# Kernel optimization log

Hardware: AMD Instinct MI355X
Metric: run time of the kernel (lower is better)

Reference implementation:

```python
import jax, jax.numpy as jnp
import numpy as np

B, T, N_MODEL, HEAD_SIZE = 8, 4096, 1024, 128


def setup_inputs() -> dict:
    key = jax.random.key(0)
    k1, k2 = jax.random.split(key)
    x = jax.random.normal(k1, (B, T, N_MODEL), dtype=jnp.float32)
    W_K = jax.random.normal(k2, (HEAD_SIZE, N_MODEL), dtype=jnp.float32) * 0.02
    return {"x": x, "W_K": W_K}


def _rope_inplace_semantics(t, cos, sin):
    """Replicates the source's in-place slice writes:
    even' = t1*cos + t2*sin  (written first)
    odd'  = -even'*sin + t2*cos  (t1 view already holds even' when read)
    """
    t1 = t[..., ::2]
    t2 = t[..., 1::2]
    even = t1 * cos + t2 * sin
    odd = -even * sin + t2 * cos
    # re-interleave: [..., half, 2] -> [..., head_size]
    return jnp.stack([even, odd], axis=-1).reshape(t.shape)


def reference(x, W_K):
    head_size = W_K.shape[0]
    T_len = x.shape[-2]
    half = head_size // 2
    # frequency-only thetas (no position index, as in source)
    thetas = jnp.power(10000.0, -(jnp.arange(half, dtype=jnp.float32) / half))
    cos = jnp.cos(thetas)
    sin = jnp.sin(thetas)

    # NOTE: source uses self.K for k, q AND v (faithful to the bug)
    k = x @ W_K.T  # [B, T, head_size]
    v = k
    k_rot = _rope_inplace_semantics(k, cos, sin)
    q_rot = k_rot  # q computed identically from K(x)

    # w[i,j] = k_i . q_j (k first, as in source einsum)
    w = jnp.einsum('bik,bjk->bij', k_rot, q_rot) * (head_size ** -0.5)
    mask = jnp.triu(jnp.full((T_len, T_len), -jnp.inf, dtype=w.dtype), k=1)
    w = jax.nn.softmax(w + mask, axis=-1)
    out = jnp.einsum('bij,bjk->bik', w, v)  # [B, T, head_size]
    return out
```

## Files before the change

### kernel.cpp

```cpp
#include <hip/hip_runtime.h>
#include <hip/hip_bf16.h>
#include <cstdint>

typedef __attribute__((ext_vector_type(8))) __bf16 bf16x8;
typedef __attribute__((ext_vector_type(4))) float f32x4;
typedef __attribute__((ext_vector_type(16))) float f32x16;

typedef const __attribute__((address_space(1))) void* as1cvp;
typedef __attribute__((address_space(3))) void* as3vp;

__device__ __forceinline__ void gload_lds16(const void* g, void* l) {
  __builtin_amdgcn_global_load_lds((as1cvp)g, (as3vp)l, 16, 0, 0);
}
__device__ __forceinline__ float readlane_f(float v, int l) {
  return __uint_as_float((uint32_t)__builtin_amdgcn_readlane((int)__float_as_uint(v), l));
}

#define KSCALE 0.3570962f
#define SMBIAS 24.0f

__device__ __forceinline__ int vperm(int p) {
  return 16 * (p >> 4) + 4 * ((p >> 3) & 1) + 8 * ((p >> 2) & 1) + (p & 3);
}

__global__ __launch_bounds__(256) void wk_convert_kernel(
    const float* __restrict__ wk, __bf16* __restrict__ wkbf) {
  int i = (blockIdx.x * 256 + threadIdx.x) * 4;
  f32x4 v = *(const f32x4*)(wk + i);
  union { __bf16 e[4]; uint64_t u; } p;
#pragma unroll
  for (int j = 0; j < 4; j++) p.e[j] = (__bf16)v[j];
  *(uint64_t*)(wkbf + i) = p.u;
}

__global__ __launch_bounds__(256, 4) void proj_rope_kernel(
    const float* __restrict__ x, const __bf16* __restrict__ wkbf,
    __bf16* __restrict__ k2, __bf16* __restrict__ vt3)
{
  __shared__ __align__(16) char psmem[40960];
  const int tid = threadIdx.x;
  const int wid = tid >> 6;
  const int lane = tid & 63;
  const int m0 = blockIdx.x * 32;
  const int wn = wid * 32;

  f32x4 acc[2][2];
#pragma unroll
  for (int i = 0; i < 2; i++)
#pragma unroll
    for (int j = 0; j < 2; j++) acc[i][j] = (f32x4)0.f;

  const int ar = tid >> 3, ac = (tid & 7) * 8;
  const float* gx0 = x + (size_t)(m0 + ar) * 1024 + ac;

  f32x4 pa0, pa1;
#define LOADA(K0) do { const float* gp = gx0 + (K0); pa0 = *(const f32x4*)gp; pa1 = *(const f32x4*)(gp + 4); } while (0)
#define WRITEA(BUF) do { \
    bf16x8 av; \
    _Pragma("unroll") for (int jj = 0; jj < 4; jj++) { av[jj] = (__bf16)pa0[jj]; av[4 + jj] = (__bf16)pa1[jj]; } \
    *(bf16x8*)((__bf16*)psmem + (BUF) * 2048 + ar * 64 + (ac ^ ((ar & 7) << 3))) = av; \
  } while (0)
#define STAGEB(BUF, K0) do { \
    _Pragma("unroll") for (int h = 0; h < 4; h++) { \
      int Lc = tid + h * 256; int row = Lc >> 3, sp = Lc & 7; \
      gload_lds16((const char*)wkbf + row * 2048 + (K0) * 2 + ((sp ^ (row & 7)) << 4), \
                  psmem + 8192 + (BUF) * 16384 + Lc * 16); \
    } } while (0)

  LOADA(0);
  STAGEB(0, 0);
  WRITEA(0);
  __syncthreads();

  for (int t = 0; t < 16; t++) {
    const int buf = t & 1;
    const bool more = (t + 1 < 16);
    if (more) { LOADA((t + 1) * 64); STAGEB(buf ^ 1, (t + 1) * 64); }
    const __bf16* As = (const __bf16*)psmem + buf * 2048;
    const __bf16* Bs = (const __bf16*)(psmem + 8192 + buf * 16384);
#pragma unroll
    for (int kk = 0; kk < 2; kk++) {
      bf16x8 afr[2], bfr[2];
#pragma unroll
      for (int mi = 0; mi < 2; mi++) {
        int row = mi * 16 + (lane & 15);
        int col = (kk * 32 + (lane >> 4) * 8) ^ ((row & 7) << 3);
        afr[mi] = *(const bf16x8*)&As[row * 64 + col];
      }
#pragma unroll
      for (int ni = 0; ni < 2; ni++) {
        int row = wn + ni * 16 + (lane & 15);
        int col = (kk * 32 + (lane >> 4) * 8) ^ ((row & 7) << 3);
        bfr[ni] = *(const bf16x8*)&Bs[row * 64 + col];
      }
#pragma unroll
      for (int mi = 0; mi < 2; mi++)
#pragma unroll
        for (int ni = 0; ni < 2; ni++)
          acc[mi][ni] = __builtin_amdgcn_mfma_f32_16x16x32_bf16(afr[mi], bfr[ni], acc[mi][ni], 0, 0, 0);
    }
    if (more) WRITEA(buf ^ 1);
    __syncthreads();
  }

  float cosv[2], sinv[2];
#pragma unroll
  for (int ni = 0; ni < 2; ni++) {
    int d = wn + ni * 16 + (lane & 15);
    float theta = exp2f((float)(d >> 1) * -0.20762050593046014f);
    cosv[ni] = cosf(theta);
    sinv[ni] = sinf(theta);
  }
  __bf16* vl = (__bf16*)psmem;
  __bf16* kl_e = (__bf16*)(psmem + 8192);
  const bool evenlane = ((lane & 1) == 0);
#pragma unroll
  for (int mi = 0; mi < 2; mi++) {
#pragma unroll
    for (int r = 0; r < 4; r++) {
      int ml = mi * 16 + (lane >> 4) * 4 + r;
#pragma unroll
      for (int ni = 0; ni < 2; ni++) {
        float val = acc[mi][ni][r];
        int d = wn + ni * 16 + (lane & 15);
        vl[ml * 128 + d] = (__bf16)val;
        float partner = __shfl_xor(val, 1);
        float e = evenlane ? val : partner;
        float o = evenlane ? partner : val;
        float ev = e * cosv[ni] + o * sinv[ni];
        float od = -ev * sinv[ni] + o * cosv[ni];
        float kr = evenlane ? ev : od;
        kl_e[ml * 128 + (d ^ ((ml & 15) << 3))] = (__bf16)(kr * KSCALE);
      }
    }
  }
  __syncthreads();
  const size_t T = blockIdx.x;
  {
    int s = tid >> 4, kvb = tid & 15;
    __bf16* kg = k2 + T * 4096 + s * 256;
#pragma unroll
    for (int h = 0; h < 2; h++) {
      int kv = kvb + h * 16;
      bf16x8 w = *(const bf16x8*)&kl_e[kv * 128 + ((s * 8) ^ ((kv & 15) << 3))];
      *(bf16x8*)(kg + kv * 8) = w;
    }
  }
  {
    int d = tid >> 1, th = tid & 1;
    __bf16* vg = vt3 + T * 4096 + d * 8;
#pragma unroll
    for (int cc = 0; cc < 2; cc++) {
      int c = 2 * th + cc;
      bf16x8 w;
#pragma unroll
      for (int jj = 0; jj < 8; jj++)
        w[jj] = vl[vperm(c * 8 + jj) * 128 + d];
      *(bf16x8*)(vg + c * 1024) = w;
    }
  }
}

__global__ __launch_bounds__(128) void attn_kernel(
    const __bf16* __restrict__ k2, const __bf16* __restrict__ vt3,
    float* __restrict__ out)
{
  __shared__ __align__(16) char smem[16512];
  const int tid = threadIdx.x;
  const int split = tid >> 6;
  const int lane = tid & 63;
  const int lo5 = lane & 31;
  const int hi = lane >> 5;
  const int b = blockIdx.x & 7;
  const int i = (int)(blockIdx.x >> 3);
  const int qb = (i < 64) ? (127 - i) : (i - 64);
  const int q0 = qb * 32;
  const int jd = qb;
  const __bf16* kt = k2 + (size_t)b * 524288;
  const __bf16* vb = vt3 + (size_t)b * 524288;

  bf16x8 qf[8];
  {
    const __bf16* qp = kt + (size_t)qb * 4096 + lo5 * 8;
#pragma unroll
    for (int ks = 0; ks < 8; ks++) qf[ks] = *(const bf16x8*)(qp + (2 * ks + hi) * 256);
  }

  f32x16 acc[4];
#pragma unroll
  for (int dt = 0; dt < 4; dt++) acc[dt] = (f32x16)0.f;
  float l_r = 0.f;

  for (int j = split; j <= jd; j += 2) {
    const __bf16* kp = kt + (size_t)j * 4096 + lo5 * 8;
    const __bf16* vp = vb + (size_t)j * 4096 + lo5 * 8;
    bf16x8 kf[8];
#pragma unroll
    for (int ks = 0; ks < 8; ks++) kf[ks] = *(const bf16x8*)(kp + (2 * ks + hi) * 256);
    bf16x8 vf0[4], vf1[4];
#pragma unroll
    for (int dt = 0; dt < 4; dt++) {
      vf0[dt] = *(const bf16x8*)(vp + hi * 1024 + dt * 256);
      vf1[dt] = *(const bf16x8*)(vp + (2 + hi) * 1024 + dt * 256);
    }
    f32x16 S = (f32x16)(-SMBIAS);
    __builtin_amdgcn_s_setprio(1);
#pragma unroll
    for (int ks = 0; ks < 8; ks++)
      S = __builtin_amdgcn_mfma_f32_32x32x16_bf16(kf[ks], qf[ks], S, 0, 0, 0);
    __builtin_amdgcn_s_setprio(0);
    if (j == jd) {
      const int kv0 = j * 32;
#pragma unroll
      for (int r = 0; r < 16; r++) {
        int kvg = kv0 + (r & 3) + 8 * (r >> 2) + 4 * hi;
        if (kvg > q0 + lo5) S[r] = -1e30f;
      }
    }
    union U { __bf16 e[8]; bf16x8 v; };
    U pk0, pk1;
    float rs = 0.f;
#pragma unroll
    for (int jj = 0; jj < 8; jj++) { float p = exp2f(S[jj]); rs += p; pk0.e[jj] = (__bf16)p; }
#pragma unroll
    for (int jj = 0; jj < 8; jj++) { float p = exp2f(S[8 + jj]); rs += p; pk1.e[jj] = (__bf16)p; }
    l_r += rs;
    __builtin_amdgcn_s_setprio(1);
#pragma unroll
    for (int dt = 0; dt < 4; dt++)
      acc[dt] = __builtin_amdgcn_mfma_f32_32x32x16_bf16(pk0.v, vf0[dt], acc[dt], 0, 0, 0);
#pragma unroll
    for (int dt = 0; dt < 4; dt++)
      acc[dt] = __builtin_amdgcn_mfma_f32_32x32x16_bf16(pk1.v, vf1[dt], acc[dt], 0, 0, 0);
    __builtin_amdgcn_s_setprio(0);
  }
  l_r += __shfl_xor(l_r, 32);

  float* mreg = (float*)smem;
  float* lbuf = (float*)(smem + 16384);
  if (split == 1) {
#pragma unroll
    for (int r = 0; r < 16; r++) {
      int ql = (r & 3) + 8 * (r >> 2) + 4 * hi;
#pragma unroll
      for (int dt = 0; dt < 4; dt++) mreg[ql * 128 + dt * 32 + lo5] = acc[dt][r];
    }
    if (lane < 32) lbuf[lane] = l_r;
  }
  __syncthreads();
  if (split == 0) {
    float invl = 1.0f / (l_r + lbuf[lo5]);
    float* ob = out + (size_t)b * 4096 * 128;
#pragma unroll
    for (int r = 0; r < 16; r++) {
      const int rb = (r & 3) + 8 * (r >> 2);
      float ivr = hi ? readlane_f(invl, rb + 4) : readlane_f(invl, rb);
      const int ql = rb + 4 * hi;
      const size_t qg = (size_t)(q0 + ql);
#pragma unroll
      for (int dt = 0; dt < 4; dt++) {
        float ov = (acc[dt][r] + mreg[ql * 128 + dt * 32 + lo5]) * ivr;
        ob[qg * 128 + dt * 32 + lo5] = ov;
      }
    }
  }
}

extern "C" void kernel_launch(void* const* d_in, const int* in_sizes, int n_in,
                              void* d_out, int out_size, void* d_ws, size_t ws_size,
                              hipStream_t stream) {
  const float* x  = (const float*)d_in[0];
  const float* wk = (const float*)d_in[1];
  __bf16* k2  = (__bf16*)d_ws;
  __bf16* vt3 = k2 + (size_t)8 * 4096 * 128;
  float* out  = (float*)d_out;
  __bf16* wkbf = (__bf16*)d_out;
  wk_convert_kernel<<<128, 256, 0, stream>>>(wk, wkbf);
  proj_rope_kernel<<<1024, 256, 0, stream>>>(x, wkbf, k2, vt3);
  attn_kernel<<<1024, 128, 0, stream>>>(k2, vt3, out);
}
```

Measured before the change: 98.15 us.

## Share K/V tiles across two query blocks via double-buffered LDS staging

The attention kernel now processes 64 query rows per workgroup (four waves: two query sub-blocks times two KV splits) and stages K and V tiles into LDS with async global-to-LDS loads, double-buffered across iterations. Each staged K/V tile is reused by both query sub-blocks, halving global K/V traffic, and the next tile is prefetched while the current one is consumed. The QK^T MFMA chain is split into two independent accumulators to shorten dependency latency. It adds a workgroup barrier per iteration and 64KB of LDS, which lowers occupancy and makes waves wait on each other.

```diff
diff --git a/kernel.cpp b/kernel.cpp
--- a/kernel.cpp
+++ b/kernel.cpp
@@ -161,29 +161,30 @@
   }
 }
 
-__global__ __launch_bounds__(128) void attn_kernel(
+__global__ __launch_bounds__(256) void attn_kernel(
     const __bf16* __restrict__ k2, const __bf16* __restrict__ vt3,
     float* __restrict__ out)
 {
-  __shared__ __align__(16) char smem[16512];
+  __shared__ __align__(16) char smem[65536];
   const int tid = threadIdx.x;
-  const int split = tid >> 6;
+  const int wid = tid >> 6;
   const int lane = tid & 63;
   const int lo5 = lane & 31;
   const int hi = lane >> 5;
   const int b = blockIdx.x & 7;
   const int i = (int)(blockIdx.x >> 3);
-  const int qb = (i < 64) ? (127 - i) : (i - 64);
-  const int q0 = qb * 32;
-  const int jd = qb;
-  const __bf16* kt = k2 + (size_t)b * 524288;
-  const __bf16* vb = vt3 + (size_t)b * 524288;
+  const int qb = (i < 32) ? (63 - i) : (i - 32);
+  const int sub = wid >> 1, split = wid & 1;
+  const int q0 = qb * 64 + sub * 32;
+  const int jd = 2 * qb + sub;
+  const char* kbc = (const char*)(k2 + (size_t)b * 524288);
+  const char* vbc = (const char*)(vt3 + (size_t)b * 524288);
 
   bf16x8 qf[8];
   {
-    const __bf16* qp = kt + (size_t)qb * 4096 + lo5 * 8;
-#pragma unroll
-    for (int ks = 0; ks < 8; ks++) qf[ks] = *(const bf16x8*)(qp + (2 * ks + hi) * 256);
+    const char* qp = kbc + (size_t)(2 * qb + sub) * 8192 + lo5 * 16;
+#pragma unroll
+    for (int ks = 0; ks < 8; ks++) qf[ks] = *(const bf16x8*)(qp + (2 * ks + hi) * 512);
   }
 
   f32x16 acc[4];
@@ -191,53 +192,78 @@
   for (int dt = 0; dt < 4; dt++) acc[dt] = (f32x16)0.f;
   float l_r = 0.f;
 
-  for (int j = split; j <= jd; j += 2) {
-    const __bf16* kp = kt + (size_t)j * 4096 + lo5 * 8;
-    const __bf16* vp = vb + (size_t)j * 4096 + lo5 * 8;
-    bf16x8 kf[8];
-#pragma unroll
-    for (int ks = 0; ks < 8; ks++) kf[ks] = *(const bf16x8*)(kp + (2 * ks + hi) * 256);
-    bf16x8 vf0[4], vf1[4];
-#pragma unroll
-    for (int dt = 0; dt < 4; dt++) {
-      vf0[dt] = *(const bf16x8*)(vp + hi * 1024 + dt * 256);
-      vf1[dt] = *(const bf16x8*)(vp + (2 + hi) * 1024 + dt * 256);
-    }
-    f32x16 S = (f32x16)(-SMBIAS);
-    __builtin_amdgcn_s_setprio(1);
-#pragma unroll
-    for (int ks = 0; ks < 8; ks++)
-      S = __builtin_amdgcn_mfma_f32_32x32x16_bf16(kf[ks], qf[ks], S, 0, 0, 0);
-    __builtin_amdgcn_s_setprio(0);
-    if (j == jd) {
-      const int kv0 = j * 32;
-#pragma unroll
-      for (int r = 0; r < 16; r++) {
-        int kvg = kv0 + (r & 3) + 8 * (r >> 2) + 4 * hi;
-        if (kvg > q0 + lo5) S[r] = -1e30f;
-      }
-    }
-    union U { __bf16 e[8]; bf16x8 v; };
-    U pk0, pk1;
-    float rs = 0.f;
-#pragma unroll
-    for (int jj = 0; jj < 8; jj++) { float p = exp2f(S[jj]); rs += p; pk0.e[jj] = (__bf16)p; }
-#pragma unroll
-    for (int jj = 0; jj < 8; jj++) { float p = exp2f(S[8 + jj]); rs += p; pk1.e[jj] = (__bf16)p; }
-    l_r += rs;
-    __builtin_amdgcn_s_setprio(1);
-#pragma unroll
-    for (int dt = 0; dt < 4; dt++)
-      acc[dt] = __builtin_amdgcn_mfma_f32_32x32x16_bf16(pk0.v, vf0[dt], acc[dt], 0, 0, 0);
-#pragma unroll
-    for (int dt = 0; dt < 4; dt++)
-      acc[dt] = __builtin_amdgcn_mfma_f32_32x32x16_bf16(pk1.v, vf1[dt], acc[dt], 0, 0, 0);
-    __builtin_amdgcn_s_setprio(0);
+#define STAGE(BSEL, JP) do { \
+    _Pragma("unroll") \
+    for (int t = 0; t < 2; t++) { \
+      const char* ks_ = kbc + (size_t)((JP) * 2 + t) * 8192; \
+      const char* vs_ = vbc + (size_t)((JP) * 2 + t) * 8192; \
+      char* dst_ = smem + (BSEL) * 32768 + t * 16384; \
+      _Pragma("unroll") \
+      for (int h = 0; h < 2; h++) { \
+        gload_lds16(ks_ + (tid + h * 256) * 16, dst_ + (tid + h * 256) * 16); \
+        gload_lds16(vs_ + (tid + h * 256) * 16, dst_ + 8192 + (tid + h * 256) * 16); \
+      } \
+    } \
+  } while (0)
+
+  const int nj = qb + 1;
+  STAGE(0, 0);
+  __syncthreads();
+
+  for (int jp = 0; jp < nj; jp++) {
+    if (jp + 1 < nj) STAGE((jp + 1) & 1, jp + 1);
+    const int j = jp * 2 + split;
+    if (j <= jd) {
+      const char* tb = smem + (jp & 1) * 32768 + split * 16384;
+      f32x16 S0 = (f32x16)(-SMBIAS), S1 = (f32x16)0.f;
+      __builtin_amdgcn_s_setprio(1);
+#pragma unroll
+      for (int ks = 0; ks < 4; ks++) {
+        bf16x8 kf = *(const bf16x8*)(tb + lo5 * 16 + (2 * ks + hi) * 512);
+        S0 = __builtin_amdgcn_mfma_f32_32x32x16_bf16(kf, qf[ks], S0, 0, 0, 0);
+      }
+#pragma unroll
+      for (int ks = 4; ks < 8; ks++) {
+        bf16x8 kf = *(const bf16x8*)(tb + lo5 * 16 + (2 * ks + hi) * 512);
+        S1 = __builtin_amdgcn_mfma_f32_32x32x16_bf16(kf, qf[ks], S1, 0, 0, 0);
+      }
+      __builtin_amdgcn_s_setprio(0);
+      f32x16 S = S0 + S1;
+      if (j == jd) {
+        const int kv0 = j * 32;
+#pragma unroll
+        for (int r = 0; r < 16; r++) {
+          int kvg = kv0 + (r & 3) + 8 * (r >> 2) + 4 * hi;
+          if (kvg > q0 + lo5) S[r] = -1e30f;
+        }
+      }
+      union U { __bf16 e[8]; bf16x8 v; };
+      U pk0, pk1;
+      float rs = 0.f;
+#pragma unroll
+      for (int jj = 0; jj < 8; jj++) { float p = exp2f(S[jj]); rs += p; pk0.e[jj] = (__bf16)p; }
+#pragma unroll
+      for (int jj = 0; jj < 8; jj++) { float p = exp2f(S[8 + jj]); rs += p; pk1.e[jj] = (__bf16)p; }
+      l_r += rs;
+      __builtin_amdgcn_s_setprio(1);
+#pragma unroll
+      for (int dt = 0; dt < 4; dt++) {
+        bf16x8 vf0 = *(const bf16x8*)(tb + 8192 + hi * 2048 + (dt * 32 + lo5) * 16);
+        acc[dt] = __builtin_amdgcn_mfma_f32_32x32x16_bf16(pk0.v, vf0, acc[dt], 0, 0, 0);
+      }
+#pragma unroll
+      for (int dt = 0; dt < 4; dt++) {
+        bf16x8 vf1 = *(const bf16x8*)(tb + 8192 + (2 + hi) * 2048 + (dt * 32 + lo5) * 16);
+        acc[dt] = __builtin_amdgcn_mfma_f32_32x32x16_bf16(pk1.v, vf1, acc[dt], 0, 0, 0);
+      }
+      __builtin_amdgcn_s_setprio(0);
+    }
+    __syncthreads();
   }
   l_r += __shfl_xor(l_r, 32);
 
-  float* mreg = (float*)smem;
-  float* lbuf = (float*)(smem + 16384);
+  float* mreg = (float*)(smem + sub * 16384);
+  float* lbuf = (float*)(smem + 32768);
   if (split == 1) {
 #pragma unroll
     for (int r = 0; r < 16; r++) {
@@ -245,11 +271,11 @@
 #pragma unroll
       for (int dt = 0; dt < 4; dt++) mreg[ql * 128 + dt * 32 + lo5] = acc[dt][r];
     }
-    if (lane < 32) lbuf[lane] = l_r;
+    if (lane < 32) lbuf[sub * 32 + lane] = l_r;
   }
   __syncthreads();
   if (split == 0) {
-    float invl = 1.0f / (l_r + lbuf[lo5]);
+    float invl = 1.0f / (l_r + lbuf[sub * 32 + lo5]);
     float* ob = out + (size_t)b * 4096 * 128;
 #pragma unroll
     for (int r = 0; r < 16; r++) {
@@ -277,5 +303,5 @@
   __bf16* wkbf = (__bf16*)d_out;
   wk_convert_kernel<<<128, 256, 0, stream>>>(wk, wkbf);
   proj_rope_kernel<<<1024, 256, 0, stream>>>(x, wkbf, k2, vt3);
-  attn_kernel<<<1024, 128, 0, stream>>>(k2, vt3, out);
-}
+  attn_kernel<<<512, 256, 0, stream>>>(k2, vt3, out);
+}
```

After: 112.6 us. 14.7% more time.

## Process two query blocks per attention workgroup to reuse K/V loads

Applied to the files above, without the earlier changes.

Each attention workgroup now handles 64 query rows as two 32-row sub-blocks that share every loaded K and V fragment, halving global K/V traffic per query. The grid shrinks from 1024 to 512 blocks and the LDS reduction buffer doubles. The QK accumulation is also split into two independent MFMA chains per sub-block to expose more instruction-level parallelism, and the setprio hints are removed. In exchange, register pressure roughly doubles (two accumulator sets and two Q fragment sets), which may lower occupancy, and the reduced block count may cause worse load balance across CUs.

```diff
diff --git a/kernel.cpp b/kernel.cpp
--- a/kernel.cpp
+++ b/kernel.cpp
@@ -165,7 +165,7 @@
     const __bf16* __restrict__ k2, const __bf16* __restrict__ vt3,
     float* __restrict__ out)
 {
-  __shared__ __align__(16) char smem[16512];
+  __shared__ __align__(16) char smem[33024];
   const int tid = threadIdx.x;
   const int split = tid >> 6;
   const int lane = tid & 63;
@@ -173,25 +173,29 @@
   const int hi = lane >> 5;
   const int b = blockIdx.x & 7;
   const int i = (int)(blockIdx.x >> 3);
-  const int qb = (i < 64) ? (127 - i) : (i - 64);
-  const int q0 = qb * 32;
-  const int jd = qb;
+  const int qc = (i < 32) ? (63 - i) : (i - 32);
+  const int q0 = qc * 64;
   const __bf16* kt = k2 + (size_t)b * 524288;
   const __bf16* vb = vt3 + (size_t)b * 524288;
 
-  bf16x8 qf[8];
+  bf16x8 qfA[8], qfB[8];
   {
-    const __bf16* qp = kt + (size_t)qb * 4096 + lo5 * 8;
-#pragma unroll
-    for (int ks = 0; ks < 8; ks++) qf[ks] = *(const bf16x8*)(qp + (2 * ks + hi) * 256);
-  }
-
-  f32x16 acc[4];
-#pragma unroll
-  for (int dt = 0; dt < 4; dt++) acc[dt] = (f32x16)0.f;
-  float l_r = 0.f;
-
-  for (int j = split; j <= jd; j += 2) {
+    const __bf16* qpA = kt + (size_t)(2 * qc) * 4096 + lo5 * 8;
+#pragma unroll
+    for (int ks = 0; ks < 8; ks++) {
+      qfA[ks] = *(const bf16x8*)(qpA + (2 * ks + hi) * 256);
+      qfB[ks] = *(const bf16x8*)(qpA + 4096 + (2 * ks + hi) * 256);
+    }
+  }
+
+  f32x16 accA[4], accB[4];
+#pragma unroll
+  for (int dt = 0; dt < 4; dt++) { accA[dt] = (f32x16)0.f; accB[dt] = (f32x16)0.f; }
+  float lA = 0.f, lB = 0.f;
+
+  const int nIter = qc + 1;
+  for (int it = 0; it < nIter; it++) {
+    const int j = 2 * it + split;
     const __bf16* kp = kt + (size_t)j * 4096 + lo5 * 8;
     const __bf16* vp = vb + (size_t)j * 4096 + lo5 * 8;
     bf16x8 kf[8];
@@ -203,64 +207,85 @@
       vf0[dt] = *(const bf16x8*)(vp + hi * 1024 + dt * 256);
       vf1[dt] = *(const bf16x8*)(vp + (2 + hi) * 1024 + dt * 256);
     }
-    f32x16 S = (f32x16)(-SMBIAS);
-    __builtin_amdgcn_s_setprio(1);
-#pragma unroll
-    for (int ks = 0; ks < 8; ks++)
-      S = __builtin_amdgcn_mfma_f32_32x32x16_bf16(kf[ks], qf[ks], S, 0, 0, 0);
-    __builtin_amdgcn_s_setprio(0);
-    if (j == jd) {
+    f32x16 SA0 = (f32x16)(-SMBIAS), SA1 = (f32x16)0.f;
+    f32x16 SB0 = (f32x16)(-SMBIAS), SB1 = (f32x16)0.f;
+#pragma unroll
+    for (int ks = 0; ks < 4; ks++) {
+      SA0 = __builtin_amdgcn_mfma_f32_32x32x16_bf16(kf[ks], qfA[ks], SA0, 0, 0, 0);
+      SB0 = __builtin_amdgcn_mfma_f32_32x32x16_bf16(kf[ks], qfB[ks], SB0, 0, 0, 0);
+    }
+#pragma unroll
+    for (int ks = 4; ks < 8; ks++) {
+      SA1 = __builtin_amdgcn_mfma_f32_32x32x16_bf16(kf[ks], qfA[ks], SA1, 0, 0, 0);
+      SB1 = __builtin_amdgcn_mfma_f32_32x32x16_bf16(kf[ks], qfB[ks], SB1, 0, 0, 0);
+    }
+    f32x16 SA = SA0 + SA1;
+    f32x16 SB = SB0 + SB1;
+    if (it == nIter - 1) {
       const int kv0 = j * 32;
 #pragma unroll
       for (int r = 0; r < 16; r++) {
         int kvg = kv0 + (r & 3) + 8 * (r >> 2) + 4 * hi;
-        if (kvg > q0 + lo5) S[r] = -1e30f;
+        if (kvg > q0 + lo5) SA[r] = -1e30f;
+        if (kvg > q0 + 32 + lo5) SB[r] = -1e30f;
       }
     }
     union U { __bf16 e[8]; bf16x8 v; };
-    U pk0, pk1;
-    float rs = 0.f;
-#pragma unroll
-    for (int jj = 0; jj < 8; jj++) { float p = exp2f(S[jj]); rs += p; pk0.e[jj] = (__bf16)p; }
-#pragma unroll
-    for (int jj = 0; jj < 8; jj++) { float p = exp2f(S[8 + jj]); rs += p; pk1.e[jj] = (__bf16)p; }
-    l_r += rs;
-    __builtin_amdgcn_s_setprio(1);
-#pragma unroll
-    for (int dt = 0; dt < 4; dt++)
-      acc[dt] = __builtin_amdgcn_mfma_f32_32x32x16_bf16(pk0.v, vf0[dt], acc[dt], 0, 0, 0);
-#pragma unroll
-    for (int dt = 0; dt < 4; dt++)
-      acc[dt] = __builtin_amdgcn_mfma_f32_32x32x16_bf16(pk1.v, vf1[dt], acc[dt], 0, 0, 0);
-    __builtin_amdgcn_s_setprio(0);
-  }
-  l_r += __shfl_xor(l_r, 32);
+    U pkA0, pkA1, pkB0, pkB1;
+    float rsA = 0.f, rsB = 0.f;
+#pragma unroll
+    for (int jj = 0; jj < 8; jj++) {
+      float pa0 = exp2f(SA[jj]);     rsA += pa0; pkA0.e[jj] = (__bf16)pa0;
+      float pa1 = exp2f(SA[8 + jj]); rsA += pa1; pkA1.e[jj] = (__bf16)pa1;
+      float pb0 = exp2f(SB[jj]);     rsB += pb0; pkB0.e[jj] = (__bf16)pb0;
+      float pb1 = exp2f(SB[8 + jj]); rsB += pb1; pkB1.e[jj] = (__bf16)pb1;
+    }
+    lA += rsA; lB += rsB;
+#pragma unroll
+    for (int dt = 0; dt < 4; dt++) {
+      accA[dt] = __builtin_amdgcn_mfma_f32_32x32x16_bf16(pkA0.v, vf0[dt], accA[dt], 0, 0, 0);
+      accB[dt] = __builtin_amdgcn_mfma_f32_32x32x16_bf16(pkB0.v, vf0[dt], accB[dt], 0, 0, 0);
+    }
+#pragma unroll
+    for (int dt = 0; dt < 4; dt++) {
+      accA[dt] = __builtin_amdgcn_mfma_f32_32x32x16_bf16(pkA1.v, vf1[dt], accA[dt], 0, 0, 0);
+      accB[dt] = __builtin_amdgcn_mfma_f32_32x32x16_bf16(pkB1.v, vf1[dt], accB[dt], 0, 0, 0);
+    }
+  }
+  lA += __shfl_xor(lA, 32);
+  lB += __shfl_xor(lB, 32);
 
   float* mreg = (float*)smem;
-  float* lbuf = (float*)(smem + 16384);
+  float* lbuf = (float*)(smem + 32768);
   if (split == 1) {
 #pragma unroll
     for (int r = 0; r < 16; r++) {
       int ql = (r & 3) + 8 * (r >> 2) + 4 * hi;
 #pragma unroll
-      for (int dt = 0; dt < 4; dt++) mreg[ql * 128 + dt * 32 + lo5] = acc[dt][r];
-    }
-    if (lane < 32) lbuf[lane] = l_r;
+      for (int dt = 0; dt < 4; dt++) {
+        mreg[ql * 128 + dt * 32 + lo5] = accA[dt][r];
+        mreg[(32 + ql) * 128 + dt * 32 + lo5] = accB[dt][r];
+      }
+    }
+    if (lane < 32) { lbuf[lane] = lA; lbuf[32 + lane] = lB; }
   }
   __syncthreads();
   if (split == 0) {
-    float invl = 1.0f / (l_r + lbuf[lo5]);
+    float invlA = 1.0f / (lA + lbuf[lo5]);
+    float invlB = 1.0f / (lB + lbuf[32 + lo5]);
     float* ob = out + (size_t)b * 4096 * 128;
 #pragma unroll
     for (int r = 0; r < 16; r++) {
       const int rb = (r & 3) + 8 * (r >> 2);
-      float ivr = hi ? readlane_f(invl, rb + 4) : readlane_f(invl, rb);
+      float ivA = hi ? readlane_f(invlA, rb + 4) : readlane_f(invlA, rb);
+      float ivB = hi ? readlane_f(invlB, rb + 4) : readlane_f(invlB, rb);
       const int ql = rb + 4 * hi;
-      const size_t qg = (size_t)(q0 + ql);
 #pragma unroll
       for (int dt = 0; dt < 4; dt++) {
-        float ov = (acc[dt][r] + mreg[ql * 128 + dt * 32 + lo5]) * ivr;
-        ob[qg * 128 + dt * 32 + lo5] = ov;
+        float ovA = (accA[dt][r] + mreg[ql * 128 + dt * 32 + lo5]) * ivA;
+        float ovB = (accB[dt][r] + mreg[(32 + ql) * 128 + dt * 32 + lo5]) * ivB;
+        ob[(size_t)(q0 + ql) * 128 + dt * 32 + lo5] = ovA;
+        ob[(size_t)(q0 + 32 + ql) * 128 + dt * 32 + lo5] = ovB;
       }
     }
   }
@@ -277,5 +302,5 @@
   __bf16* wkbf = (__bf16*)d_out;
   wk_convert_kernel<<<128, 256, 0, stream>>>(wk, wkbf);
   proj_rope_kernel<<<1024, 256, 0, stream>>>(x, wkbf, k2, vt3);
-  attn_kernel<<<1024, 128, 0, stream>>>(k2, vt3, out);
-}
+  attn_kernel<<<512, 128, 0, stream>>>(k2, vt3, out);
+}
```

After: 122.4 us. +24.7%, slower.
